# Kernel optimization log

Hardware: AMD Instinct MI355X
Metric: run time of the kernel (lower is better)

The kernel has to match this reference:

```python
import jax, jax.numpy as jnp
import numpy as np

B, DIM, H, W = 128, 640, 10, 10
M = H * W


def setup_inputs() -> dict:
    key = jax.random.key(0)
    x = jax.random.normal(key, (B, DIM, M), dtype=jnp.float32)
    # learned temperature parameter, init = log(1 / (2*h*w)), shape (1, 1)
    t = jnp.log(1.0 / (2 * H * W) * jnp.ones((1, 1), dtype=jnp.float32))
    return {"x": x, "t": t}


def reference(x, t):
    # x: [B, dim, M], t: [1, 1] temperature (log-scale)
    dim = x.shape[1]
    # Gram matrix x x^T: [B, dim, dim]
    xxT = jnp.einsum('bdm,bem->bde', x, x)
    # I_M.bmm(x_pow2*I) and (x_pow2*I).bmm(I_M) are just diagonal broadcasts
    d = jnp.diagonal(xxT, axis1=1, axis2=2)  # [B, dim]
    dcov = d[:, None, :] + d[:, :, None] - 2.0 * xxT
    dcov = jnp.maximum(dcov, 1e-4)
    dcov = jnp.sqrt(jnp.exp(t) * dcov + 1e-5)
    # double centering: dcov.bmm(I_M)/dim == row means, I_M.bmm(dcov)/dim == col means
    row_mean = jnp.mean(dcov, axis=2, keepdims=True)   # [B, dim, 1]
    col_mean = jnp.mean(dcov, axis=1, keepdims=True)   # [B, 1, dim]
    tot_mean = jnp.mean(dcov, axis=(1, 2), keepdims=True)  # [B, 1, 1]
    out = dcov - row_mean - col_mean + tot_mean
    return out.reshape(out.shape[0], dim * dim)
```

## Files before the change

### kernel.cpp

```cpp
#include <hip/hip_runtime.h>
#include <cmath>

#define NB    128
#define DIM_  640
#define MM    100
#define XHR   128
#define LDK   136
#define TFS   68
#define TTS   66

#define NWG   (NB * 55)
#define CPX   (NWG / 8)

typedef _Float16 half8 __attribute__((ext_vector_type(8)));
typedef float f32x4 __attribute__((ext_vector_type(4)));

__device__ inline void decode_bp(int bid, int& b, int& p) {
    const int dec = (bid & 7) * CPX + (bid >> 3);
    b = dec / 55;
    p = dec - b * 55;
}

__global__ __launch_bounds__(256) void prep_xh(const float* __restrict__ x,
                                               _Float16* __restrict__ xh,
                                               float* __restrict__ d) {
    const int row  = blockIdx.x * 4 + (threadIdx.x >> 6);
    const int lane = threadIdx.x & 63;
    const float* xr = x + (size_t)row * MM;
    float2 v = make_float2(0.f, 0.f);
    if (lane < 50) v = *(const float2*)(xr + 2 * lane);
    const _Float16 h0 = (_Float16)v.x, h1 = (_Float16)v.y;
    const float a0 = (float)h0, a1 = (float)h1;
    float acc = a0 * a0 + a1 * a1;
    union { _Float16 h[2]; unsigned u; } pk;
    pk.h[0] = h0; pk.h[1] = h1;
    *(unsigned*)(xh + (size_t)row * XHR + 2 * lane) = pk.u;
    #pragma unroll
    for (int off = 32; off; off >>= 1) acc += __shfl_down(acc, off, 64);
    if (lane == 0) d[row] = acc;
}

__device__ inline void stage_xh(const _Float16* __restrict__ src,
                                _Float16* __restrict__ lds, int tid) {
    #pragma unroll
    for (int i = 0; i < 4; ++i) {
        const int idx = tid + i * 256;
        const int row = idx >> 4;
        const int m   = idx & 15;
        *(half8*)(lds + row * LDK + m * 8) = *(const half8*)(src + (size_t)row * XHR + m * 8);
    }
}

__global__ __launch_bounds__(256) void bdc_sums(
        const _Float16* __restrict__ xh, const float* __restrict__ d,
        const float* __restrict__ t, float* __restrict__ r2) {
    __shared__ alignas(16) _Float16 As[64 * LDK];
    __shared__ alignas(16) _Float16 Bs[64 * LDK];
    __shared__ float rowacc[64];
    __shared__ float colacc[64];

    int b, p;
    decode_bp(blockIdx.x, b, p);
    int it = 0, rem = p;
    while (rem >= 10 - it) { rem -= 10 - it; ++it; }
    const int jt = it + rem;
    const bool diag = (it == jt);

    const int tid = threadIdx.x;
    const int wave = tid >> 6;
    const int lane = tid & 63;
    const int l16  = lane & 15;
    const int quad = lane >> 4;
    const int rowhalf = wave >> 1;
    const int colhalf = wave & 1;

    if (tid < 64)  rowacc[tid] = 0.f;
    else if (tid < 128) colacc[tid - 64] = 0.f;

    const _Float16* xb = xh + (size_t)b * DIM_ * XHR;
    stage_xh(xb + (size_t)(it * 64) * XHR, As, tid);
    if (!diag) stage_xh(xb + (size_t)(jt * 64) * XHR, Bs, tid);

    const float expt = expf(t[0]);
    const float* db = d + b * DIM_;
    const int rbase = it * 64 + rowhalf * 32;
    const int cbase = jt * 64 + colhalf * 32;
    float dr[2][4];
    #pragma unroll
    for (int ti = 0; ti < 2; ++ti)
        #pragma unroll
        for (int r = 0; r < 4; ++r)
            dr[ti][r] = db[rbase + ti * 16 + quad * 4 + r];
    const float dcv[2] = { db[cbase + l16], db[cbase + 16 + l16] };

    __syncthreads();

    const _Float16* Bp = diag ? As : Bs;
    f32x4 acc[2][2] = {};
    #pragma unroll
    for (int kk = 0; kk < 4; ++kk) {
        const int k = kk * 32 + quad * 8;
        half8 a0 = *(const half8*)(&As[(rowhalf * 32 + l16) * LDK + k]);
        half8 a1 = *(const half8*)(&As[(rowhalf * 32 + 16 + l16) * LDK + k]);
        half8 b0 = *(const half8*)(&Bp[(colhalf * 32 + l16) * LDK + k]);
        half8 b1 = *(const half8*)(&Bp[(colhalf * 32 + 16 + l16) * LDK + k]);
        acc[0][0] = __builtin_amdgcn_mfma_f32_16x16x32_f16(a0, b0, acc[0][0], 0, 0, 0);
        acc[0][1] = __builtin_amdgcn_mfma_f32_16x16x32_f16(a0, b1, acc[0][1], 0, 0, 0);
        acc[1][0] = __builtin_amdgcn_mfma_f32_16x16x32_f16(a1, b0, acc[1][0], 0, 0, 0);
        acc[1][1] = __builtin_amdgcn_mfma_f32_16x16x32_f16(a1, b1, acc[1][1], 0, 0, 0);
    }

    float cp0 = 0.f, cp1 = 0.f;
    #pragma unroll
    for (int ti = 0; ti < 2; ++ti) {
        #pragma unroll
        for (int r = 0; r < 4; ++r) {
            const int gi = rbase + ti * 16 + quad * 4 + r;
            float raw0 = dr[ti][r] + dcv[0] - 2.0f * acc[ti][0][r];
            raw0 = (gi == cbase + l16) ? 1e-4f : fmaxf(raw0, 1e-4f);
            const float v0 = sqrtf(expt * raw0 + 1e-5f);
            float raw1 = dr[ti][r] + dcv[1] - 2.0f * acc[ti][1][r];
            raw1 = (gi == cbase + 16 + l16) ? 1e-4f : fmaxf(raw1, 1e-4f);
            const float v1 = sqrtf(expt * raw1 + 1e-5f);
            cp0 += v0; cp1 += v1;
            float s = v0 + v1;
            s += __shfl_xor(s, 1, 64);
            s += __shfl_xor(s, 2, 64);
            s += __shfl_xor(s, 4, 64);
            s += __shfl_xor(s, 8, 64);
            if (l16 == 0)
                atomicAdd(&rowacc[rowhalf * 32 + ti * 16 + quad * 4 + r], s);
        }
    }
    cp0 += __shfl_xor(cp0, 16, 64); cp0 += __shfl_xor(cp0, 32, 64);
    cp1 += __shfl_xor(cp1, 16, 64); cp1 += __shfl_xor(cp1, 32, 64);
    if (quad == 0) {
        atomicAdd(&colacc[colhalf * 32 + l16],      cp0);
        atomicAdd(&colacc[colhalf * 32 + 16 + l16], cp1);
    }

    __syncthreads();

    if (tid < 64) {
        r2[((size_t)b * 10 + jt) * DIM_ + it * 64 + tid] = rowacc[tid];
        if (!diag)
            r2[((size_t)b * 10 + it) * DIM_ + jt * 64 + tid] = colacc[tid];
    }
}

__global__ __launch_bounds__(256) void bdc_out(
        const _Float16* __restrict__ xh, const float* __restrict__ d,
        const float* __restrict__ t, const float* __restrict__ r2,
        float* __restrict__ out) {
    __shared__ alignas(16) char uni[35200];
    _Float16* As = (_Float16*)uni;
    _Float16* Bs = (_Float16*)(uni + 17408);
    float* Tf = (float*)uni;
    float* Tt = (float*)(uni + 17408);
    __shared__ float rm_s[DIM_];
    __shared__ float wred[4];

    int b, p;
    decode_bp(blockIdx.x, b, p);
    int it = 0, rem = p;
    while (rem >= 10 - it) { rem -= 10 - it; ++it; }
    const int jt = it + rem;
    const bool diag = (it == jt);

    const int tid  = threadIdx.x;
    const int wave = tid >> 6;
    const int lane = tid & 63;
    const int l16  = lane & 15;
    const int quad = lane >> 4;
    const int rowhalf = wave >> 1;
    const int colhalf = wave & 1;

    const _Float16* xb = xh + (size_t)b * DIM_ * XHR;
    stage_xh(xb + (size_t)(it * 64) * XHR, As, tid);
    if (!diag) stage_xh(xb + (size_t)(jt * 64) * XHR, Bs, tid);

    const float* rb = r2 + (size_t)b * 10 * DIM_;
    float tpart = 0.f;
    for (int i = tid; i < DIM_; i += 256) {
        float s = 0.f;
        #pragma unroll
        for (int ss = 0; ss < 10; ++ss) s += rb[ss * DIM_ + i];
        rm_s[i] = s * (1.0f / 640.0f);
        tpart += s;
    }
    #pragma unroll
    for (int off = 32; off; off >>= 1) tpart += __shfl_xor(tpart, off, 64);
    if (lane == 0) wred[wave] = tpart;

    const float expt = expf(t[0]);
    const float* db = d + b * DIM_;
    const int rbase = it * 64 + rowhalf * 32;
    const int cbase = jt * 64 + colhalf * 32;
    float dr[2][4];
    #pragma unroll
    for (int ti = 0; ti < 2; ++ti)
        #pragma unroll
        for (int r = 0; r < 4; ++r)
            dr[ti][r] = db[rbase + ti * 16 + quad * 4 + r];
    const float dcv[2] = { db[cbase + l16], db[cbase + 16 + l16] };

    __syncthreads();
    const float tot = (wred[0] + wred[1] + wred[2] + wred[3]) * (1.0f / 409600.0f);

    const _Float16* Bp = diag ? As : Bs;
    f32x4 acc[2][2] = {};
    #pragma unroll
    for (int kk = 0; kk < 4; ++kk) {
        const int k = kk * 32 + quad * 8;
        half8 a0 = *(const half8*)(&As[(rowhalf * 32 + l16) * LDK + k]);
        half8 a1 = *(const half8*)(&As[(rowhalf * 32 + 16 + l16) * LDK + k]);
        half8 b0 = *(const half8*)(&Bp[(colhalf * 32 + l16) * LDK + k]);
        half8 b1 = *(const half8*)(&Bp[(colhalf * 32 + 16 + l16) * LDK + k]);
        acc[0][0] = __builtin_amdgcn_mfma_f32_16x16x32_f16(a0, b0, acc[0][0], 0, 0, 0);
        acc[0][1] = __builtin_amdgcn_mfma_f32_16x16x32_f16(a0, b1, acc[0][1], 0, 0, 0);
        acc[1][0] = __builtin_amdgcn_mfma_f32_16x16x32_f16(a1, b0, acc[1][0], 0, 0, 0);
        acc[1][1] = __builtin_amdgcn_mfma_f32_16x16x32_f16(a1, b1, acc[1][1], 0, 0, 0);
    }

    float o[2][4][2];
    #pragma unroll
    for (int ti = 0; ti < 2; ++ti)
        #pragma unroll
        for (int r = 0; r < 4; ++r) {
            const int gi = rbase + ti * 16 + quad * 4 + r;
            const float rowterm = tot - rm_s[gi];
            #pragma unroll
            for (int tj = 0; tj < 2; ++tj) {
                const int gj = cbase + tj * 16 + l16;
                float raw = dr[ti][r] + dcv[tj] - 2.0f * acc[ti][tj][r];
                raw = (gi == gj) ? 1e-4f : fmaxf(raw, 1e-4f);
                o[ti][r][tj] = sqrtf(expt * raw + 1e-5f) + rowterm - rm_s[gj];
            }
        }

    __syncthreads();

    #pragma unroll
    for (int ti = 0; ti < 2; ++ti)
        #pragma unroll
        for (int r = 0; r < 4; ++r) {
            const int rowl = rowhalf * 32 + ti * 16 + quad * 4 + r;
            #pragma unroll
            for (int tj = 0; tj < 2; ++tj) {
                const int coll = colhalf * 32 + tj * 16 + l16;
                Tf[rowl * TFS + coll] = o[ti][r][tj];
                if (!diag)
                    Tt[coll * TTS + (rowl ^ ((l16 & 3) << 2))] = o[ti][r][tj];
            }
        }

    __syncthreads();

    float* ob = out + (size_t)b * DIM_ * DIM_;
    #pragma unroll
    for (int k4 = 0; k4 < 4; ++k4) {
        const int w  = tid + k4 * 256;
        const int rr = w >> 4;
        const int c4 = (w & 15) * 4;
        const f32x4 v = *(const f32x4*)(&Tf[rr * TFS + c4]);
        *(f32x4*)(ob + (size_t)(it * 64 + rr) * DIM_ + jt * 64 + c4) = v;
    }
    if (!diag) {
        #pragma unroll
        for (int k4 = 0; k4 < 4; ++k4) {
            const int w  = tid + k4 * 256;
            const int rr = w >> 4;
            const int c4 = (w & 15) * 4;
            const int cc = c4 ^ ((rr & 3) << 2);
            const float2 p0 = *(const float2*)(&Tt[rr * TTS + cc]);
            const float2 p1 = *(const float2*)(&Tt[rr * TTS + cc + 2]);
            const f32x4 v = { p0.x, p0.y, p1.x, p1.y };
            *(f32x4*)(ob + (size_t)(jt * 64 + rr) * DIM_ + it * 64 + c4) = v;
        }
    }
}

extern "C" void kernel_launch(void* const* d_in, const int* in_sizes, int n_in,
                              void* d_out, int out_size, void* d_ws, size_t ws_size,
                              hipStream_t stream) {
    const float* x = (const float*)d_in[0];
    const float* t = (const float*)d_in[1];
    float* out = (float*)d_out;

    char* ws = (char*)d_ws;
    _Float16* xh = (_Float16*)ws;
    float*    d  = (float*)(ws + 20971520);
    float*    r2 = (float*)(ws + 20971520 + 327680);

    prep_xh<<<dim3(NB * DIM_ / 4), dim3(256), 0, stream>>>(x, xh, d);
    bdc_sums<<<dim3(NWG), dim3(256), 0, stream>>>(xh, d, t, r2);
    bdc_out<<<dim3(NWG), dim3(256), 0, stream>>>(xh, d, t, r2, out);
}
```

Measured before the change: 283.5 us.

## Accumulate row means and totals with global atomics; use nontemporal output stores

bdc_sums no longer writes per-tile partial row sums to a 10-slice buffer. It reduces each tile's row and column sums through a padded LDS scratch area that reuses the As buffer, then atomically adds them into a per-batch row-mean array and a per-batch total that prep_xh zeroes first. bdc_out now reads the finished means and total directly instead of summing 10 slices and doing a block-wide reduction. The large output writes switch to nontemporal stores to reduce cache pollution. This trades shuffle chains and LDS atomics for global atomics, which may contend and makes float summation order nondeterministic.

```diff
diff --git a/kernel.cpp b/kernel.cpp
--- a/kernel.cpp
+++ b/kernel.cpp
@@ -8,6 +8,8 @@
 #define LDK   136
 #define TFS   68
 #define TTS   66
+#define RSS   34
+#define CSS   10
 
 #define NWG   (NB * 55)
 #define CPX   (NWG / 8)
@@ -23,7 +25,12 @@
 
 __global__ __launch_bounds__(256) void prep_xh(const float* __restrict__ x,
                                                _Float16* __restrict__ xh,
-                                               float* __restrict__ d) {
+                                               float* __restrict__ d,
+                                               float* __restrict__ rmz) {
+    if (blockIdx.x < 321) {
+        const int z = blockIdx.x * 256 + threadIdx.x;
+        if (z < 82048) rmz[z] = 0.f;
+    }
     const int row  = blockIdx.x * 4 + (threadIdx.x >> 6);
     const int lane = threadIdx.x & 63;
     const float* xr = x + (size_t)row * MM;
@@ -53,11 +60,12 @@
 
 __global__ __launch_bounds__(256) void bdc_sums(
         const _Float16* __restrict__ xh, const float* __restrict__ d,
-        const float* __restrict__ t, float* __restrict__ r2) {
+        const float* __restrict__ t, float* __restrict__ rm,
+        float* __restrict__ tot) {
     __shared__ alignas(16) _Float16 As[64 * LDK];
     __shared__ alignas(16) _Float16 Bs[64 * LDK];
-    __shared__ float rowacc[64];
-    __shared__ float colacc[64];
+    float* rsum = (float*)As;
+    float* csum = (float*)As + 64 * RSS;
 
     int b, p;
     decode_bp(blockIdx.x, b, p);
@@ -73,9 +81,6 @@
     const int quad = lane >> 4;
     const int rowhalf = wave >> 1;
     const int colhalf = wave & 1;
-
-    if (tid < 64)  rowacc[tid] = 0.f;
-    else if (tid < 128) colacc[tid - 64] = 0.f;
 
     const _Float16* xb = xh + (size_t)b * DIM_ * XHR;
     stage_xh(xb + (size_t)(it * 64) * XHR, As, tid);
@@ -110,6 +115,7 @@
         acc[1][1] = __builtin_amdgcn_mfma_f32_16x16x32_f16(a1, b1, acc[1][1], 0, 0, 0);
     }
 
+    float s2[2][4];
     float cp0 = 0.f, cp1 = 0.f;
     #pragma unroll
     for (int ti = 0; ti < 2; ++ti) {
@@ -122,43 +128,52 @@
             float raw1 = dr[ti][r] + dcv[1] - 2.0f * acc[ti][1][r];
             raw1 = (gi == cbase + 16 + l16) ? 1e-4f : fmaxf(raw1, 1e-4f);
             const float v1 = sqrtf(expt * raw1 + 1e-5f);
+            s2[ti][r] = v0 + v1;
             cp0 += v0; cp1 += v1;
-            float s = v0 + v1;
-            s += __shfl_xor(s, 1, 64);
-            s += __shfl_xor(s, 2, 64);
-            s += __shfl_xor(s, 4, 64);
-            s += __shfl_xor(s, 8, 64);
-            if (l16 == 0)
-                atomicAdd(&rowacc[rowhalf * 32 + ti * 16 + quad * 4 + r], s);
         }
     }
-    cp0 += __shfl_xor(cp0, 16, 64); cp0 += __shfl_xor(cp0, 32, 64);
-    cp1 += __shfl_xor(cp1, 16, 64); cp1 += __shfl_xor(cp1, 32, 64);
-    if (quad == 0) {
-        atomicAdd(&colacc[colhalf * 32 + l16],      cp0);
-        atomicAdd(&colacc[colhalf * 32 + 16 + l16], cp1);
-    }
+
+    __syncthreads();
+
+    #pragma unroll
+    for (int ti = 0; ti < 2; ++ti)
+        #pragma unroll
+        for (int r = 0; r < 4; ++r)
+            rsum[(rowhalf * 32 + ti * 16 + quad * 4 + r) * RSS + colhalf * 16 + l16] = s2[ti][r];
+    csum[(colhalf * 32 + l16) * CSS + rowhalf * 4 + quad]      = cp0;
+    csum[(colhalf * 32 + 16 + l16) * CSS + rowhalf * 4 + quad] = cp1;
 
     __syncthreads();
 
     if (tid < 64) {
-        r2[((size_t)b * 10 + jt) * DIM_ + it * 64 + tid] = rowacc[tid];
-        if (!diag)
-            r2[((size_t)b * 10 + it) * DIM_ + jt * 64 + tid] = colacc[tid];
+        float rt = 0.f;
+        const float2* rp = (const float2*)(rsum + tid * RSS);
+        #pragma unroll
+        for (int k = 0; k < 16; ++k) { const float2 u = rp[k]; rt += u.x + u.y; }
+        atomicAdd(&rm[b * DIM_ + it * 64 + tid], rt);
+        float ts = rt;
+        #pragma unroll
+        for (int off = 1; off < 64; off <<= 1) ts += __shfl_xor(ts, off, 64);
+        if (tid == 0) atomicAdd(&tot[b], diag ? ts : 2.0f * ts);
+    } else if (tid < 128 && !diag) {
+        const int c = tid - 64;
+        float ct = 0.f;
+        #pragma unroll
+        for (int s = 0; s < 8; ++s) ct += csum[c * CSS + s];
+        atomicAdd(&rm[b * DIM_ + jt * 64 + c], ct);
     }
 }
 
 __global__ __launch_bounds__(256) void bdc_out(
         const _Float16* __restrict__ xh, const float* __restrict__ d,
-        const float* __restrict__ t, const float* __restrict__ r2,
-        float* __restrict__ out) {
+        const float* __restrict__ t, const float* __restrict__ rm,
+        const float* __restrict__ tot_g, float* __restrict__ out) {
     __shared__ alignas(16) char uni[35200];
     _Float16* As = (_Float16*)uni;
     _Float16* Bs = (_Float16*)(uni + 17408);
     float* Tf = (float*)uni;
     float* Tt = (float*)(uni + 17408);
     __shared__ float rm_s[DIM_];
-    __shared__ float wred[4];
 
     int b, p;
     decode_bp(blockIdx.x, b, p);
@@ -179,18 +194,9 @@
     stage_xh(xb + (size_t)(it * 64) * XHR, As, tid);
     if (!diag) stage_xh(xb + (size_t)(jt * 64) * XHR, Bs, tid);
 
-    const float* rb = r2 + (size_t)b * 10 * DIM_;
-    float tpart = 0.f;
-    for (int i = tid; i < DIM_; i += 256) {
-        float s = 0.f;
-        #pragma unroll
-        for (int ss = 0; ss < 10; ++ss) s += rb[ss * DIM_ + i];
-        rm_s[i] = s * (1.0f / 640.0f);
-        tpart += s;
-    }
-    #pragma unroll
-    for (int off = 32; off; off >>= 1) tpart += __shfl_xor(tpart, off, 64);
-    if (lane == 0) wred[wave] = tpart;
+    const float* rmg = rm + (size_t)b * DIM_;
+    for (int i = tid; i < DIM_; i += 256) rm_s[i] = rmg[i] * (1.0f / 640.0f);
+    const float tot = tot_g[b] * (1.0f / 409600.0f);
 
     const float expt = expf(t[0]);
     const float* db = d + b * DIM_;
@@ -205,7 +211,6 @@
     const float dcv[2] = { db[cbase + l16], db[cbase + 16 + l16] };
 
     __syncthreads();
-    const float tot = (wred[0] + wred[1] + wred[2] + wred[3]) * (1.0f / 409600.0f);
 
     const _Float16* Bp = diag ? As : Bs;
     f32x4 acc[2][2] = {};
@@ -263,7 +268,7 @@
         const int rr = w >> 4;
         const int c4 = (w & 15) * 4;
         const f32x4 v = *(const f32x4*)(&Tf[rr * TFS + c4]);
-        *(f32x4*)(ob + (size_t)(it * 64 + rr) * DIM_ + jt * 64 + c4) = v;
+        __builtin_nontemporal_store(v, (f32x4*)(ob + (size_t)(it * 64 + rr) * DIM_ + jt * 64 + c4));
     }
     if (!diag) {
         #pragma unroll
@@ -275,7 +280,7 @@
             const float2 p0 = *(const float2*)(&Tt[rr * TTS + cc]);
             const float2 p1 = *(const float2*)(&Tt[rr * TTS + cc + 2]);
             const f32x4 v = { p0.x, p0.y, p1.x, p1.y };
-            *(f32x4*)(ob + (size_t)(jt * 64 + rr) * DIM_ + it * 64 + c4) = v;
+            __builtin_nontemporal_store(v, (f32x4*)(ob + (size_t)(jt * 64 + rr) * DIM_ + it * 64 + c4));
         }
     }
 }
@@ -290,9 +295,10 @@
     char* ws = (char*)d_ws;
     _Float16* xh = (_Float16*)ws;
     float*    d  = (float*)(ws + 20971520);
-    float*    r2 = (float*)(ws + 20971520 + 327680);
-
-    prep_xh<<<dim3(NB * DIM_ / 4), dim3(256), 0, stream>>>(x, xh, d);
-    bdc_sums<<<dim3(NWG), dim3(256), 0, stream>>>(xh, d, t, r2);
-    bdc_out<<<dim3(NWG), dim3(256), 0, stream>>>(xh, d, t, r2, out);
-}
+    float*    rm = (float*)(ws + 20971520 + 327680);
+    float*    tot= (float*)(ws + 20971520 + 2 * 327680);
+
+    prep_xh<<<dim3(NB * DIM_ / 4), dim3(256), 0, stream>>>(x, xh, d, rm);
+    bdc_sums<<<dim3(NWG), dim3(256), 0, stream>>>(xh, d, t, rm, tot);
+    bdc_out<<<dim3(NWG), dim3(256), 0, stream>>>(xh, d, t, rm, tot, out);
+}
```

After: 275.5 us. 2.8% less time.
